# Optimization experiments

Measured on AMD Instinct MI355X. Metric: run time of the kernel, lower is better.

The kernel has to match this reference:

```python
import jax, jax.numpy as jnp
import numpy as np

B, J, H, OUT_LEN = 16, 2048, 2048, 128  # seq_len J must equal hidden_dim H
HDIM = H // OUT_LEN  # 16


def setup_inputs() -> dict:
    key = jax.random.key(0)
    k_vec, k_wq, k_wk, k_wv = jax.random.split(key, 4)
    scale = 1.0 / np.sqrt(H)  # keep projections well-scaled (xavier-like)
    return {
        "vec": jax.random.normal(k_vec, (B, J, H), dtype=jnp.float32),
        "wq_w": jax.random.normal(k_wq, (OUT_LEN, H), dtype=jnp.float32) * scale,
        "wq_b": jnp.ones((OUT_LEN,), dtype=jnp.float32),
        "wk_w": jax.random.normal(k_wk, (H, H), dtype=jnp.float32) * scale,
        "wk_b": jnp.ones((H,), dtype=jnp.float32),
        "wv_w": jax.random.normal(k_wv, (HDIM, H), dtype=jnp.float32) * scale,
        "wv_b": jnp.ones((HDIM,), dtype=jnp.float32),
    }


def reference(vec, wq_w, wq_b, wk_w, wk_b, wv_w, wv_b):
    # Projections (nn.Linear: x @ W.T + b)
    q = vec @ wq_w.T + wq_b          # [B, J, out_len]
    k = vec @ wk_w.T + wk_b          # [B, J, H]
    v = vec @ wv_w.T + wv_b          # [B, J, hdim]
    # attn[b, i, h] = sum_j q[b, j, i] * k[b, j, h]  -> [B, out_len, H]
    attn = jnp.einsum('bji,bjk->bij', q, k)
    attn = jax.nn.softmax(jnp.tanh(attn), axis=-1)
    # ret[b, i, d] = sum_j attn[b, i, j] * v[b, j, d]  (requires H == J)
    ret = jnp.einsum('bij,bjk->bik', attn, v)  # [B, out_len, hdim]
    return ret
```

## Files before the change

### kernel.cpp

```cpp
#include <hip/hip_runtime.h>
#include <hip/hip_bf16.h>
#include <math.h>

#define Bn   16
#define Jn   2048
#define Hn   2048
#define OUTn 128
#define HDn  16

#define KC      64
#define NCHUNK  (Hn / KC)
#define A_UNITS 512
#define B_UNITS 1280
#define WPK_CHUNK_BYTES (2 * B_UNITS * 16)

typedef __attribute__((ext_vector_type(8))) short bf16x8_t;
typedef __attribute__((ext_vector_type(4))) float f32x4_t;

typedef __attribute__((address_space(1))) const void gvoid_t;
typedef __attribute__((address_space(3))) void lvoid_t;

__device__ __forceinline__ unsigned short f2bf(float x) {
  unsigned u = __builtin_bit_cast(unsigned, x);
  unsigned r = (u + 0x7fffu + ((u >> 16) & 1u)) >> 16;
  return (unsigned short)r;
}
__device__ __forceinline__ float bf2f(unsigned short h) {
  unsigned u = ((unsigned)h) << 16;
  return __builtin_bit_cast(float, u);
}

__global__ __launch_bounds__(256) void prep1_kernel(const float* __restrict__ wk_w,
                                                    const float* __restrict__ wk_b,
                                                    float* __restrict__ ws) {
  const int blk = blockIdx.x;
  const int tid = threadIdx.x;
  if (blk < 256) {
    const int h0 = blk * 8;
    for (int c = tid; c < Hn; c += 256) {
      float s = 0.f;
#pragma unroll
      for (int h = 0; h < 8; ++h) s += wk_w[(size_t)(h0 + h) * Hn + c];
      atomicAdd(&ws[8 + c], s);
    }
  } else {
    __shared__ float red[256];
    float s = 0.f;
    for (int h = tid; h < Hn; h += 256) s += wk_b[h];
    red[tid] = s;
    __syncthreads();
    for (int off = 128; off > 0; off >>= 1) {
      if (tid < off) red[tid] += red[tid + off];
      __syncthreads();
    }
    if (tid == 0) ws[0] = red[0];
  }
}

__global__ __launch_bounds__(256) void prep2_kernel(const float* __restrict__ wq_w,
                                                    const float* __restrict__ wv_w,
                                                    const float* __restrict__ wsc,
                                                    uint4* __restrict__ wpk) {
  const int id = blockIdx.x * 256 + threadIdx.x;
  const int chunk = id / B_UNITS;
  const int u     = id % B_UNITS;
  const int kblk  = u / 640;
  const int u2    = u % 640;
  const int nt    = u2 >> 6;
  const int g     = (u2 >> 4) & 3;
  const int n16   = u2 & 15;
  const int n     = nt * 16 + n16;
  const int k     = chunk * KC + kblk * 32 + g * 8;

  float x[8];
  if (n < OUTn) {
    const float* s = wq_w + (size_t)n * Hn + k;
#pragma unroll
    for (int i = 0; i < 8; ++i) x[i] = s[i];
  } else if (n < OUTn + HDn) {
    const float* s = wv_w + (size_t)(n - OUTn) * Hn + k;
#pragma unroll
    for (int i = 0; i < 8; ++i) x[i] = s[i];
  } else if (n == OUTn + HDn) {
    const float* s = wsc + 8 + k;
#pragma unroll
    for (int i = 0; i < 8; ++i) x[i] = s[i];
  } else {
#pragma unroll
    for (int i = 0; i < 8; ++i) x[i] = 0.f;
  }

  unsigned short hi[8], lo[8];
#pragma unroll
  for (int i = 0; i < 8; ++i) {
    hi[i] = f2bf(x[i]);
    lo[i] = f2bf(x[i] - bf2f(hi[i]));
  }
  uint4 uh, ul;
  uh.x = (unsigned)hi[0] | ((unsigned)hi[1] << 16);
  uh.y = (unsigned)hi[2] | ((unsigned)hi[3] << 16);
  uh.z = (unsigned)hi[4] | ((unsigned)hi[5] << 16);
  uh.w = (unsigned)hi[6] | ((unsigned)hi[7] << 16);
  ul.x = (unsigned)lo[0] | ((unsigned)lo[1] << 16);
  ul.y = (unsigned)lo[2] | ((unsigned)lo[3] << 16);
  ul.z = (unsigned)lo[4] | ((unsigned)lo[5] << 16);
  ul.w = (unsigned)lo[6] | ((unsigned)lo[7] << 16);
  wpk[(size_t)(chunk * 2 + 0) * B_UNITS + u] = uh;
  wpk[(size_t)(chunk * 2 + 1) * B_UNITS + u] = ul;
}

__global__ __launch_bounds__(256, 2) void proj_kernel(
    const float* __restrict__ vec,
    const float* __restrict__ wq_b,
    const float* __restrict__ wv_b,
    const float* __restrict__ wsc,
    const uint4* __restrict__ wpk,
    float* __restrict__ qT,
    float* __restrict__ ksum,
    float* __restrict__ vout)
{
  __shared__ uint4 As[2 * A_UNITS];
  __shared__ uint4 Bs[2 * B_UNITS];

  const int tid  = threadIdx.x;
  const int lane = tid & 63;
  const int w    = tid >> 6;
  const int wm   = w >> 1;
  const int wn   = w & 1;
  const int b    = blockIdx.x >> 5;
  const int j0   = (blockIdx.x & 31) * 64;

  const float* vecb = vec + (size_t)b * Jn * Hn;
  const bf16x8_t* As8 = (const bf16x8_t*)As;
  const bf16x8_t* Bs8 = (const bf16x8_t*)Bs;

  f32x4_t acc[2][5];
#pragma unroll
  for (int mi = 0; mi < 2; ++mi)
#pragma unroll
    for (int ni = 0; ni < 5; ++ni) acc[mi][ni] = (f32x4_t){0.f, 0.f, 0.f, 0.f};

  for (int chunk = 0; chunk < NCHUNK; ++chunk) {
    const int k0 = chunk * KC;
#pragma unroll
    for (int rep = 0; rep < 2; ++rep) {
      const int u    = tid + rep * 256;
      const int kblk = u >> 8;
      const int mt   = (u >> 6) & 3;
      const int g    = (u >> 4) & 3;
      const int m    = u & 15;
      const float* src = vecb + (size_t)(j0 + mt * 16 + m) * Hn + k0 + kblk * 32 + g * 8;
      const float4 a0 = *(const float4*)src;
      const float4 a1 = *(const float4*)(src + 4);
      float x[8] = {a0.x, a0.y, a0.z, a0.w, a1.x, a1.y, a1.z, a1.w};
      unsigned short hi[8], lo[8];
#pragma unroll
      for (int i = 0; i < 8; ++i) {
        hi[i] = f2bf(x[i]);
        lo[i] = f2bf(x[i] - bf2f(hi[i]));
      }
      uint4 uh, ul;
      uh.x = (unsigned)hi[0] | ((unsigned)hi[1] << 16);
      uh.y = (unsigned)hi[2] | ((unsigned)hi[3] << 16);
      uh.z = (unsigned)hi[4] | ((unsigned)hi[5] << 16);
      uh.w = (unsigned)hi[6] | ((unsigned)hi[7] << 16);
      ul.x = (unsigned)lo[0] | ((unsigned)lo[1] << 16);
      ul.y = (unsigned)lo[2] | ((unsigned)lo[3] << 16);
      ul.z = (unsigned)lo[4] | ((unsigned)lo[5] << 16);
      ul.w = (unsigned)lo[6] | ((unsigned)lo[7] << 16);
      As[u]           = uh;
      As[A_UNITS + u] = ul;
    }
    {
      const char* gbase = (const char*)wpk + (size_t)chunk * WPK_CHUNK_BYTES + (size_t)lane * 16;
#pragma unroll
      for (int i = 0; i < 10; ++i) {
        const int q = w + i * 4;
        __builtin_amdgcn_global_load_lds((gvoid_t*)(gbase + q * 1024),
                                         (lvoid_t*)&Bs[q * 64], 16, 0, 0);
      }
    }
    __syncthreads();

#pragma unroll
    for (int kblk = 0; kblk < 2; ++kblk) {
      bf16x8_t bh[5], bl[5];
#pragma unroll
      for (int ni = 0; ni < 5; ++ni) {
        const int idx = (kblk * 10 + wn * 5 + ni) * 64 + lane;
        bh[ni] = Bs8[idx];
        bl[ni] = Bs8[B_UNITS + idx];
      }
#pragma unroll
      for (int mi = 0; mi < 2; ++mi) {
        const int aidx = (kblk * 4 + wm * 2 + mi) * 64 + lane;
        const bf16x8_t ah = As8[aidx];
        const bf16x8_t al = As8[A_UNITS + aidx];
#pragma unroll
        for (int ni = 0; ni < 5; ++ni) {
          acc[mi][ni] = __builtin_amdgcn_mfma_f32_16x16x32_bf16(ah, bh[ni], acc[mi][ni], 0, 0, 0);
          acc[mi][ni] = __builtin_amdgcn_mfma_f32_16x16x32_bf16(ah, bl[ni], acc[mi][ni], 0, 0, 0);
          acc[mi][ni] = __builtin_amdgcn_mfma_f32_16x16x32_bf16(al, bh[ni], acc[mi][ni], 0, 0, 0);
        }
      }
    }
    __syncthreads();
  }

  const float wkb = wsc[0];
  const int col16 = lane & 15;
  const int rbase = (lane >> 4) * 4;
#pragma unroll
  for (int mi = 0; mi < 2; ++mi) {
#pragma unroll
    for (int ni = 0; ni < 5; ++ni) {
      const int n  = (wn * 5 + ni) * 16 + col16;
      const int jg = j0 + (wm * 2 + mi) * 16 + rbase;
      const f32x4_t c = acc[mi][ni];
      if (n < OUTn) {
        const float bias = wq_b[n];
        float4 o = {c[0] + bias, c[1] + bias, c[2] + bias, c[3] + bias};
        *(float4*)(qT + ((size_t)(b * OUTn + n)) * Jn + jg) = o;
      } else if (n < OUTn + HDn) {
        const int d = n - OUTn;
        const float bias = wv_b[d];
#pragma unroll
        for (int r = 0; r < 4; ++r)
          vout[((size_t)b * Jn + jg + r) * HDn + d] = c[r] + bias;
      } else if (n == OUTn + HDn) {
#pragma unroll
        for (int r = 0; r < 4; ++r)
          ksum[(size_t)b * Jn + jg + r] = c[r] + wkb;
      }
    }
  }
}

__global__ __launch_bounds__(256) void attn_kernel(
    const float* __restrict__ qT,
    const float* __restrict__ ksum,
    const float* __restrict__ v,
    float* __restrict__ out)
{
  const int bi  = blockIdx.x;
  const int b   = bi >> 7;
  const int tid = threadIdx.x;
  const float* qrow = qT + (size_t)bi * Jn;
  const float* ks   = ksum + (size_t)b * Jn;
  const float* vb   = v + (size_t)b * Jn * HDn;

  float Z = 0.f;
  float racc[HDn];
#pragma unroll
  for (int d = 0; d < HDn; ++d) racc[d] = 0.f;

  for (int j = tid; j < Jn; j += 256) {
    const float attnv = qrow[j] * ks[j];
    const float e2x = __expf(attnv + attnv);
    const float t   = 1.f - 2.f / (e2x + 1.f);
    const float p   = __expf(t);
    Z += p;
    const float4* vr = (const float4*)(vb + (size_t)j * HDn);
    const float4 v0 = vr[0], v1 = vr[1], v2 = vr[2], v3 = vr[3];
    racc[0]  += p * v0.x; racc[1]  += p * v0.y; racc[2]  += p * v0.z; racc[3]  += p * v0.w;
    racc[4]  += p * v1.x; racc[5]  += p * v1.y; racc[6]  += p * v1.z; racc[7]  += p * v1.w;
    racc[8]  += p * v2.x; racc[9]  += p * v2.y; racc[10] += p * v2.z; racc[11] += p * v2.w;
    racc[12] += p * v3.x; racc[13] += p * v3.y; racc[14] += p * v3.z; racc[15] += p * v3.w;
  }
#pragma unroll
  for (int off = 32; off > 0; off >>= 1) {
    Z += __shfl_down(Z, off);
#pragma unroll
    for (int d = 0; d < HDn; ++d) racc[d] += __shfl_down(racc[d], off);
  }
  __shared__ float red[4][HDn + 1];
  const int wv = tid >> 6;
  if ((tid & 63) == 0) {
    red[wv][0] = Z;
#pragma unroll
    for (int d = 0; d < HDn; ++d) red[wv][1 + d] = racc[d];
  }
  __syncthreads();
  if (tid < HDn + 1) {
    red[0][tid] = red[0][tid] + red[1][tid] + red[2][tid] + red[3][tid];
  }
  __syncthreads();
  if (tid < HDn) {
    out[(size_t)bi * HDn + tid] = red[0][1 + tid] / red[0][0];
  }
}

extern "C" void kernel_launch(void* const* d_in, const int* in_sizes, int n_in,
                              void* d_out, int out_size, void* d_ws, size_t ws_size,
                              hipStream_t stream) {
  const float* vec  = (const float*)d_in[0];
  const float* wq_w = (const float*)d_in[1];
  const float* wq_b = (const float*)d_in[2];
  const float* wk_w = (const float*)d_in[3];
  const float* wk_b = (const float*)d_in[4];
  const float* wv_w = (const float*)d_in[5];
  const float* wv_b = (const float*)d_in[6];

  float* ws   = (float*)d_ws;
  uint4* wpk  = (uint4*)(ws + 4096);
  float* qT   = ws + 4096 + (NCHUNK * 2 * B_UNITS * 4);
  float* ksum = qT + (size_t)Bn * OUTn * Jn;
  float* vout = ksum + (size_t)Bn * Jn;
  float* out  = (float*)d_out;

  hipMemsetAsync(ws, 0, (8 + Hn) * sizeof(float), stream);
  prep1_kernel<<<257, 256, 0, stream>>>(wk_w, wk_b, ws);
  prep2_kernel<<<(NCHUNK * B_UNITS) / 256, 256, 0, stream>>>(wq_w, wv_w, ws, wpk);
  proj_kernel<<<Bn * (Jn / 64), 256, 0, stream>>>(vec, wq_b, wv_b, ws, wpk,
                                                  qT, ksum, vout);
  attn_kernel<<<Bn * OUTn, 256, 0, stream>>>(qT, ksum, vout, out);
}
```

Measured before the change: 450.4 us.

## Fuse tanh-softmax-attention epilogue into projection kernel with partial-sum finalize

Removes the qT/ksum/v round trip through global memory and the separate attention kernel. Each projection tile now applies tanh, exp and the V-weighted accumulation in its epilogue and writes per-tile partial sums, which a small finalize kernel reduces and normalizes. The prep step also replaces column atomics with per-block partial rows that prep2 reduces, and the memset is dropped. In exchange, epilogue register pressure rises and softmax runs without max subtraction (safe because tanh bounds the logits).

```diff
diff --git a/kernel.cpp b/kernel.cpp
--- a/kernel.cpp
+++ b/kernel.cpp
@@ -13,6 +13,10 @@
 #define A_UNITS 512
 #define B_UNITS 1280
 #define WPK_CHUNK_BYTES (2 * B_UNITS * 16)
+
+#define WS_PART1 2048
+#define WS_WPK   (WS_PART1 + 256 * 2048)
+#define WS_PART  (WS_WPK + NCHUNK * 2 * B_UNITS * 4)
 
 typedef __attribute__((ext_vector_type(8))) short bf16x8_t;
 typedef __attribute__((ext_vector_type(4))) float f32x4_t;
@@ -37,12 +41,19 @@
   const int tid = threadIdx.x;
   if (blk < 256) {
     const int h0 = blk * 8;
-    for (int c = tid; c < Hn; c += 256) {
-      float s = 0.f;
-#pragma unroll
-      for (int h = 0; h < 8; ++h) s += wk_w[(size_t)(h0 + h) * Hn + c];
-      atomicAdd(&ws[8 + c], s);
-    }
+    const int c0 = tid * 8;
+    float a[8] = {0.f, 0.f, 0.f, 0.f, 0.f, 0.f, 0.f, 0.f};
+#pragma unroll
+    for (int h = 0; h < 8; ++h) {
+      const float* row = wk_w + (size_t)(h0 + h) * Hn + c0;
+      const float4 u = *(const float4*)row;
+      const float4 v = *(const float4*)(row + 4);
+      a[0] += u.x; a[1] += u.y; a[2] += u.z; a[3] += u.w;
+      a[4] += v.x; a[5] += v.y; a[6] += v.z; a[7] += v.w;
+    }
+    float* dst = ws + WS_PART1 + (size_t)blk * Hn + c0;
+    *(float4*)dst       = make_float4(a[0], a[1], a[2], a[3]);
+    *(float4*)(dst + 4) = make_float4(a[4], a[5], a[6], a[7]);
   } else {
     __shared__ float red[256];
     float s = 0.f;
@@ -59,7 +70,7 @@
 
 __global__ __launch_bounds__(256) void prep2_kernel(const float* __restrict__ wq_w,
                                                     const float* __restrict__ wv_w,
-                                                    const float* __restrict__ wsc,
+                                                    const float* __restrict__ ws,
                                                     uint4* __restrict__ wpk) {
   const int id = blockIdx.x * 256 + threadIdx.x;
   const int chunk = id / B_UNITS;
@@ -82,9 +93,16 @@
 #pragma unroll
     for (int i = 0; i < 8; ++i) x[i] = s[i];
   } else if (n == OUTn + HDn) {
-    const float* s = wsc + 8 + k;
-#pragma unroll
-    for (int i = 0; i < 8; ++i) x[i] = s[i];
+#pragma unroll
+    for (int i = 0; i < 8; ++i) x[i] = 0.f;
+    const float* p1 = ws + WS_PART1 + k;
+    for (int p = 0; p < 256; ++p) {
+      const float4 a = *(const float4*)p1;
+      const float4 b = *(const float4*)(p1 + 4);
+      x[0] += a.x; x[1] += a.y; x[2] += a.z; x[3] += a.w;
+      x[4] += b.x; x[5] += b.y; x[6] += b.z; x[7] += b.w;
+      p1 += Hn;
+    }
   } else {
 #pragma unroll
     for (int i = 0; i < 8; ++i) x[i] = 0.f;
@@ -115,20 +133,21 @@
     const float* __restrict__ wv_b,
     const float* __restrict__ wsc,
     const uint4* __restrict__ wpk,
-    float* __restrict__ qT,
-    float* __restrict__ ksum,
-    float* __restrict__ vout)
+    float* __restrict__ part)
 {
   __shared__ uint4 As[2 * A_UNITS];
   __shared__ uint4 Bs[2 * B_UNITS];
 
-  const int tid  = threadIdx.x;
-  const int lane = tid & 63;
-  const int w    = tid >> 6;
-  const int wm   = w >> 1;
-  const int wn   = w & 1;
-  const int b    = blockIdx.x >> 5;
-  const int j0   = (blockIdx.x & 31) * 64;
+  const int tid   = threadIdx.x;
+  const int lane  = tid & 63;
+  const int w     = tid >> 6;
+  const int wm    = w >> 1;
+  const int wn    = w & 1;
+  const int b     = blockIdx.x >> 5;
+  const int jt    = blockIdx.x & 31;
+  const int j0    = jt * 64;
+  const int col16 = lane & 15;
+  const int rbase = (lane >> 4) * 4;
 
   const float* vecb = vec + (size_t)b * Jn * Hn;
   const bf16x8_t* As8 = (const bf16x8_t*)As;
@@ -208,86 +227,119 @@
   }
 
   const float wkb = wsc[0];
-  const int col16 = lane & 15;
-  const int rbase = (lane >> 4) * 4;
+  float* ks_s = (float*)&As[0];
+  float* vt   = ks_s + 64;
+  float* epi  = (float*)&Bs[0];
+
+  if (wn == 1) {
+    const float vb_ = wv_b[col16];
+#pragma unroll
+    for (int mi = 0; mi < 2; ++mi) {
+      const f32x4_t c = acc[mi][3];
+#pragma unroll
+      for (int r = 0; r < 4; ++r) {
+        const int j = (wm * 2 + mi) * 16 + rbase + r;
+        vt[j * 20 + col16] = c[r] + vb_;
+      }
+    }
+    if (col16 == 0) {
+#pragma unroll
+      for (int mi = 0; mi < 2; ++mi) {
+        const f32x4_t c = acc[mi][4];
+#pragma unroll
+        for (int r = 0; r < 4; ++r) {
+          const int j = (wm * 2 + mi) * 16 + rbase + r;
+          ks_s[j] = c[r] + wkb;
+        }
+      }
+    }
+  }
+  __syncthreads();
+
+  const int NCOL = wn ? 3 : 5;
+  float qb[5];
+  for (int ni = 0; ni < NCOL; ++ni) qb[ni] = wq_b[(wn * 5 + ni) * 16 + col16];
+
+  float pz[5] = {0.f, 0.f, 0.f, 0.f, 0.f};
+  float po[5][16];
+#pragma unroll
+  for (int ni = 0; ni < 5; ++ni)
+#pragma unroll
+    for (int d = 0; d < 16; ++d) po[ni][d] = 0.f;
+
 #pragma unroll
   for (int mi = 0; mi < 2; ++mi) {
 #pragma unroll
-    for (int ni = 0; ni < 5; ++ni) {
-      const int n  = (wn * 5 + ni) * 16 + col16;
-      const int jg = j0 + (wm * 2 + mi) * 16 + rbase;
-      const f32x4_t c = acc[mi][ni];
-      if (n < OUTn) {
-        const float bias = wq_b[n];
-        float4 o = {c[0] + bias, c[1] + bias, c[2] + bias, c[3] + bias};
-        *(float4*)(qT + ((size_t)(b * OUTn + n)) * Jn + jg) = o;
-      } else if (n < OUTn + HDn) {
-        const int d = n - OUTn;
-        const float bias = wv_b[d];
-#pragma unroll
-        for (int r = 0; r < 4; ++r)
-          vout[((size_t)b * Jn + jg + r) * HDn + d] = c[r] + bias;
-      } else if (n == OUTn + HDn) {
-#pragma unroll
-        for (int r = 0; r < 4; ++r)
-          ksum[(size_t)b * Jn + jg + r] = c[r] + wkb;
-      }
-    }
-  }
-}
-
-__global__ __launch_bounds__(256) void attn_kernel(
-    const float* __restrict__ qT,
-    const float* __restrict__ ksum,
-    const float* __restrict__ v,
-    float* __restrict__ out)
-{
-  const int bi  = blockIdx.x;
-  const int b   = bi >> 7;
-  const int tid = threadIdx.x;
-  const float* qrow = qT + (size_t)bi * Jn;
-  const float* ks   = ksum + (size_t)b * Jn;
-  const float* vb   = v + (size_t)b * Jn * HDn;
-
-  float Z = 0.f;
-  float racc[HDn];
-#pragma unroll
-  for (int d = 0; d < HDn; ++d) racc[d] = 0.f;
-
-  for (int j = tid; j < Jn; j += 256) {
-    const float attnv = qrow[j] * ks[j];
-    const float e2x = __expf(attnv + attnv);
-    const float t   = 1.f - 2.f / (e2x + 1.f);
-    const float p   = __expf(t);
-    Z += p;
-    const float4* vr = (const float4*)(vb + (size_t)j * HDn);
-    const float4 v0 = vr[0], v1 = vr[1], v2 = vr[2], v3 = vr[3];
-    racc[0]  += p * v0.x; racc[1]  += p * v0.y; racc[2]  += p * v0.z; racc[3]  += p * v0.w;
-    racc[4]  += p * v1.x; racc[5]  += p * v1.y; racc[6]  += p * v1.z; racc[7]  += p * v1.w;
-    racc[8]  += p * v2.x; racc[9]  += p * v2.y; racc[10] += p * v2.z; racc[11] += p * v2.w;
-    racc[12] += p * v3.x; racc[13] += p * v3.y; racc[14] += p * v3.z; racc[15] += p * v3.w;
-  }
-#pragma unroll
-  for (int off = 32; off > 0; off >>= 1) {
-    Z += __shfl_down(Z, off);
-#pragma unroll
-    for (int d = 0; d < HDn; ++d) racc[d] += __shfl_down(racc[d], off);
-  }
-  __shared__ float red[4][HDn + 1];
-  const int wv = tid >> 6;
-  if ((tid & 63) == 0) {
-    red[wv][0] = Z;
-#pragma unroll
-    for (int d = 0; d < HDn; ++d) red[wv][1 + d] = racc[d];
+    for (int r = 0; r < 4; ++r) {
+      const int j = (wm * 2 + mi) * 16 + rbase + r;
+      const float ksj = ks_s[j];
+      const float4 v0 = *(const float4*)&vt[j * 20];
+      const float4 v1 = *(const float4*)&vt[j * 20 + 4];
+      const float4 v2 = *(const float4*)&vt[j * 20 + 8];
+      const float4 v3 = *(const float4*)&vt[j * 20 + 12];
+      for (int ni = 0; ni < NCOL; ++ni) {
+        const float q   = acc[mi][ni][r] + qb[ni];
+        const float e2x = __expf(2.f * q * ksj);
+        const float t   = 1.f - 2.f / (e2x + 1.f);
+        const float p   = __expf(t);
+        pz[ni] += p;
+        po[ni][0]  += p * v0.x; po[ni][1]  += p * v0.y; po[ni][2]  += p * v0.z; po[ni][3]  += p * v0.w;
+        po[ni][4]  += p * v1.x; po[ni][5]  += p * v1.y; po[ni][6]  += p * v1.z; po[ni][7]  += p * v1.w;
+        po[ni][8]  += p * v2.x; po[ni][9]  += p * v2.y; po[ni][10] += p * v2.z; po[ni][11] += p * v2.w;
+        po[ni][12] += p * v3.x; po[ni][13] += p * v3.y; po[ni][14] += p * v3.z; po[ni][15] += p * v3.w;
+      }
+    }
+  }
+  for (int ni = 0; ni < NCOL; ++ni) {
+    pz[ni] += __shfl_xor(pz[ni], 16);
+    pz[ni] += __shfl_xor(pz[ni], 32);
+#pragma unroll
+    for (int d = 0; d < 16; ++d) {
+      po[ni][d] += __shfl_xor(po[ni][d], 16);
+      po[ni][d] += __shfl_xor(po[ni][d], 32);
+    }
+  }
+  if (wm == 0 && lane < 16) {
+    for (int ni = 0; ni < NCOL; ++ni) {
+      const int n = (wn * 5 + ni) * 16 + lane;
+      epi[n * 18 + 16] = pz[ni];
+#pragma unroll
+      for (int d = 0; d < 16; ++d) epi[n * 18 + d] = po[ni][d];
+    }
   }
   __syncthreads();
-  if (tid < HDn + 1) {
-    red[0][tid] = red[0][tid] + red[1][tid] + red[2][tid] + red[3][tid];
+  if (wm == 1 && lane < 16) {
+    for (int ni = 0; ni < NCOL; ++ni) {
+      const int n = (wn * 5 + ni) * 16 + lane;
+      epi[n * 18 + 16] += pz[ni];
+#pragma unroll
+      for (int d = 0; d < 16; ++d) epi[n * 18 + d] += po[ni][d];
+    }
   }
   __syncthreads();
-  if (tid < HDn) {
-    out[(size_t)bi * HDn + tid] = red[0][1 + tid] / red[0][0];
-  }
+  float* pout = part + ((size_t)(b * 32 + jt) * 128) * 17;
+  for (int idx = tid; idx < 128 * 17; idx += 256)
+    pout[idx] = epi[(idx / 17) * 18 + (idx % 17)];
+}
+
+__global__ __launch_bounds__(256) void finalize_kernel(const float* __restrict__ part,
+                                                       float* __restrict__ out) {
+  const int gid = blockIdx.x * 256 + threadIdx.x;
+  const float* p = part + (size_t)(gid >> 7) * 32 * 128 * 17 + (size_t)(gid & 127) * 17;
+  float z = 0.f;
+  float o[16];
+#pragma unroll
+  for (int d = 0; d < 16; ++d) o[d] = 0.f;
+  for (int jt = 0; jt < 32; ++jt) {
+    const float* pp = p + (size_t)jt * 128 * 17;
+    z += pp[16];
+#pragma unroll
+    for (int d = 0; d < 16; ++d) o[d] += pp[d];
+  }
+  const float inv = 1.f / z;
+  float* dst = out + (size_t)gid * 16;
+#pragma unroll
+  for (int d = 0; d < 16; ++d) dst[d] = o[d] * inv;
 }
 
 extern "C" void kernel_launch(void* const* d_in, const int* in_sizes, int n_in,
@@ -302,16 +354,12 @@
   const float* wv_b = (const float*)d_in[6];
 
   float* ws   = (float*)d_ws;
-  uint4* wpk  = (uint4*)(ws + 4096);
-  float* qT   = ws + 4096 + (NCHUNK * 2 * B_UNITS * 4);
-  float* ksum = qT + (size_t)Bn * OUTn * Jn;
-  float* vout = ksum + (size_t)Bn * Jn;
+  uint4* wpk  = (uint4*)(ws + WS_WPK);
+  float* part = ws + WS_PART;
   float* out  = (float*)d_out;
 
-  hipMemsetAsync(ws, 0, (8 + Hn) * sizeof(float), stream);
   prep1_kernel<<<257, 256, 0, stream>>>(wk_w, wk_b, ws);
   prep2_kernel<<<(NCHUNK * B_UNITS) / 256, 256, 0, stream>>>(wq_w, wv_w, ws, wpk);
-  proj_kernel<<<Bn * (Jn / 64), 256, 0, stream>>>(vec, wq_b, wv_b, ws, wpk,
-                                                  qT, ksum, vout);
-  attn_kernel<<<Bn * OUTn, 256, 0, stream>>>(qT, ksum, vout, out);
-}
+  proj_kernel<<<Bn * (Jn / 64), 256, 0, stream>>>(vec, wq_b, wv_b, ws, wpk, part);
+  finalize_kernel<<<8, 256, 0, stream>>>(part, out);
+}
```

After: 632.7 us. 1.4x slower.
